# Kernel tuning notes

Measured on AMD Instinct MI355X. Metric: run time of the kernel, lower is better.

## Reference

```python
import jax, jax.numpy as jnp
import numpy as np

N_NODES = 50000
N_EDGES = 800000
IN_DIM = 128
OUT_DIM = 64


def setup_inputs() -> dict:
    key = jax.random.key(0)
    k1, k2, k3, k4, k5 = jax.random.split(key, 5)
    x = jax.random.normal(k1, (N_NODES, IN_DIM), dtype=jnp.float32)
    # Glorot-uniform-ish init for the GCN weight (weight_variable_glorot)
    limit = np.sqrt(6.0 / (IN_DIM + OUT_DIM)).astype(np.float32)
    weight = jax.random.uniform(k2, (IN_DIM, OUT_DIM), dtype=jnp.float32,
                                minval=-limit, maxval=limit)
    adj_row = jax.random.randint(k3, (N_EDGES,), 0, N_NODES, dtype=jnp.int32)
    adj_col = jax.random.randint(k4, (N_EDGES,), 0, N_NODES, dtype=jnp.int32)
    adj_val = jax.random.uniform(k5, (N_EDGES,), dtype=jnp.float32)
    return {"x": x, "weight": weight, "adj_row": adj_row,
            "adj_col": adj_col, "adj_val": adj_val}


def reference(x, weight, adj_row, adj_col, adj_val):
    # x: [N, F_in], weight: [F_in, F_out]; dropout=0.0 (default) is identity.
    xw = jnp.matmul(x, weight)                      # [N, F_out] dense GEMM
    # spmm(adj, xw) with adj in COO: gather neighbor feats, scale, scatter-add
    msg = adj_val[:, None] * xw[adj_col]            # [E, F_out]
    agg = jax.ops.segment_sum(msg, adj_row, num_segments=x.shape[0])  # [N, F_out]
    return jax.nn.relu(agg)
```

## Files before the change

kernel.cpp:

```cpp
#include <hip/hip_runtime.h>

#define IN_DIM 128
#define OUT_DIM 64
#define PADK 136
#define RB 128
#define RBSH 7
#define CAPB 2560
#define AB2 256

typedef float f32x4 __attribute__((ext_vector_type(4)));
typedef short bf16x8 __attribute__((ext_vector_type(8)));

__device__ __forceinline__ unsigned short f2bf(float f) {
    unsigned u = __float_as_uint(f);
    return (unsigned short)((u + 0x7FFFu + ((u >> 16) & 1u)) >> 16);
}
__device__ __forceinline__ float bf2f(unsigned short h) {
    return __uint_as_float((unsigned)h << 16);
}

__device__ __forceinline__ void gemm_body(const float* __restrict__ x,
                                          const float* __restrict__ w,
                                          unsigned short* __restrict__ xwb,
                                          int N, int blk,
                                          unsigned short* lds) {
    unsigned short* Bhi = lds;
    unsigned short* Blo = lds + 64 * PADK;

    const int t = threadIdx.x;
    const int r0 = blk * 64;

    {
        const int c = t >> 2;
        const int kb = (t & 3) * 32;
        for (int k4 = 0; k4 < 32; k4 += 4) {
            ushort4 h, l;
            float v0 = w[(kb + k4 + 0) * OUT_DIM + c];
            float v1 = w[(kb + k4 + 1) * OUT_DIM + c];
            float v2 = w[(kb + k4 + 2) * OUT_DIM + c];
            float v3 = w[(kb + k4 + 3) * OUT_DIM + c];
            h.x = f2bf(v0); l.x = f2bf(v0 - bf2f(h.x));
            h.y = f2bf(v1); l.y = f2bf(v1 - bf2f(h.y));
            h.z = f2bf(v2); l.z = f2bf(v2 - bf2f(h.z));
            h.w = f2bf(v3); l.w = f2bf(v3 - bf2f(h.w));
            *(ushort4*)&Bhi[c * PADK + kb + k4] = h;
            *(ushort4*)&Blo[c * PADK + kb + k4] = l;
        }
    }

    const int lane = t & 63;
    const int wv = t >> 6;
    const int m = lane & 15;
    const int quad = lane >> 4;

    int row = r0 + wv * 16 + m; if (row >= N) row = N - 1;
    const float4* xr = (const float4*)(x + (size_t)row * IN_DIM);
    bf16x8 ahi[4], alo[4];
#pragma unroll
    for (int ks = 0; ks < 4; ++ks) {
        const float4 v0 = xr[ks * 8 + quad * 2];
        const float4 v1 = xr[ks * 8 + quad * 2 + 1];
        float f[8] = {v0.x, v0.y, v0.z, v0.w, v1.x, v1.y, v1.z, v1.w};
        bf16x8 h8, l8;
#pragma unroll
        for (int i = 0; i < 8; ++i) {
            const unsigned short h = f2bf(f[i]);
            h8[i] = (short)h;
            l8[i] = (short)f2bf(f[i] - bf2f(h));
        }
        ahi[ks] = h8; alo[ks] = l8;
    }
    __syncthreads();

#pragma unroll
    for (int ct = 0; ct < 4; ++ct) {
        f32x4 acc = {0.f, 0.f, 0.f, 0.f};
#pragma unroll
        for (int ks = 0; ks < 4; ++ks) {
            const int off = (ct * 16 + m) * PADK + ks * 32 + quad * 8;
            bf16x8 bh = *(const bf16x8*)&Bhi[off];
            bf16x8 bl = *(const bf16x8*)&Blo[off];
            acc = __builtin_amdgcn_mfma_f32_16x16x32_bf16(alo[ks], bh, acc, 0, 0, 0);
            acc = __builtin_amdgcn_mfma_f32_16x16x32_bf16(ahi[ks], bl, acc, 0, 0, 0);
            acc = __builtin_amdgcn_mfma_f32_16x16x32_bf16(ahi[ks], bh, acc, 0, 0, 0);
        }
#pragma unroll
        for (int i = 0; i < 4; ++i) {
            const int r = r0 + wv * 16 + quad * 4 + i;
            if (r < N) xwb[(size_t)r * OUT_DIM + ct * 16 + m] = f2bf(acc[i]);
        }
    }
}

__device__ __forceinline__ void afill_body(
        const int* __restrict__ arow, const int* __restrict__ acol,
        const float* __restrict__ aval, int* __restrict__ pcur,
        int* __restrict__ ocount, uint4* __restrict__ olist,
        uint2* __restrict__ payload, int E, int NB, int chunk, int blk,
        int* ldsi) {
    int* cnt  = ldsi;
    int* base = ldsi + 512;
    const int t = threadIdx.x;
    const int lo = blk * chunk;
    const int hi = min(E, lo + chunk);
    if (lo >= hi) return;
    const int len = hi - lo;
    const int n4  = len >> 2;
    const int4*   ar4 = (const int4*)(arow + lo);
    const int4*   ac4 = (const int4*)(acol + lo);
    const float4* av4 = (const float4*)(aval + lo);

    for (int i = t; i < NB; i += 256) cnt[i] = 0;
    __syncthreads();

    for (int j = t; j < n4; j += 256) {
        const int4 r = ar4[j];
        atomicAdd(&cnt[r.x >> RBSH], 1);
        atomicAdd(&cnt[r.y >> RBSH], 1);
        atomicAdd(&cnt[r.z >> RBSH], 1);
        atomicAdd(&cnt[r.w >> RBSH], 1);
    }
    for (int e = lo + (n4 << 2) + t; e < hi; e += 256)
        atomicAdd(&cnt[arow[e] >> RBSH], 1);
    __syncthreads();

    for (int i = t; i < NB; i += 256) {
        const int c = cnt[i];
        base[i] = c ? atomicAdd(&pcur[i], c) : 0;
        cnt[i] = 0;
    }
    __syncthreads();

#define AF_EMIT(RR, CC, VV) do {                                              \
        const int b_ = (RR) >> RBSH;                                          \
        const int slot_ = base[b_] + atomicAdd(&cnt[b_], 1);                  \
        const unsigned w0_ = (unsigned)(CC) |                                 \
                             ((unsigned)((RR) & (RB - 1)) << 16);             \
        const unsigned w1_ = __float_as_uint(VV);                             \
        if (slot_ < CAPB) {                                                   \
            payload[(size_t)b_ * CAPB + slot_] = make_uint2(w0_, w1_);        \
        } else {                                                              \
            const int oi_ = atomicAdd(ocount, 1);                             \
            olist[oi_] = make_uint4((unsigned)(RR), (unsigned)(CC), w1_, 0u); \
        }                                                                     \
    } while (0)

    for (int j = t; j < n4; j += 256) {
        const int4   r = ar4[j];
        const int4   c = ac4[j];
        const float4 v = av4[j];
        AF_EMIT(r.x, c.x, v.x);
        AF_EMIT(r.y, c.y, v.y);
        AF_EMIT(r.z, c.z, v.z);
        AF_EMIT(r.w, c.w, v.w);
    }
    for (int e = lo + (n4 << 2) + t; e < hi; e += 256)
        AF_EMIT(arow[e], acol[e], aval[e]);
#undef AF_EMIT
}

__global__ __launch_bounds__(256) void gemm_afill(
        const float* __restrict__ x, const float* __restrict__ w,
        unsigned short* __restrict__ xwb, int N,
        const int* __restrict__ arow, const int* __restrict__ acol,
        const float* __restrict__ aval, int* __restrict__ pcur,
        int* __restrict__ ocount, uint4* __restrict__ olist,
        uint2* __restrict__ payload, int E, int NB, int chunk) {
    __shared__ unsigned short LB[2 * 64 * PADK];
    if ((int)blockIdx.x < AB2) {
        afill_body(arow, acol, aval, pcur, ocount, olist, payload, E, NB,
                   chunk, blockIdx.x, (int*)LB);
    } else {
        gemm_body(x, w, xwb, N, blockIdx.x - AB2, LB);
    }
}

__global__ __launch_bounds__(256) void gemm_only(const float* __restrict__ x,
                                                 const float* __restrict__ w,
                                                 unsigned short* __restrict__ xwb,
                                                 int N) {
    __shared__ unsigned short LB[2 * 64 * PADK];
    gemm_body(x, w, xwb, N, blockIdx.x, LB);
}

__global__ __launch_bounds__(512) void bagg6(
        const int* __restrict__ pcur, const uint2* __restrict__ payload,
        const unsigned short* __restrict__ xwb, float* __restrict__ out, int N,
        const int* __restrict__ ocount, const uint4* __restrict__ olist) {
    __shared__ uint2 stage[CAPB];
    __shared__ int binc[RB];
    __shared__ int bins[RB + 1];
    __shared__ int pl[RB];
    __shared__ int hsum[2];
    const int t = threadIdx.x;
    const int lane = t & 63;
    const int wv = t >> 6;
    const int b = blockIdx.x;
    const int r0 = b << RBSH;

    const int cnt = min(pcur[b], CAPB);
    if (t < RB) { binc[t] = 0; pl[t] = 0; }
    __syncthreads();

    const uint2* pay = payload + (size_t)b * CAPB;
    for (int i = t; i < cnt; i += 512)
        atomicAdd(&binc[(pay[i].x >> 16) & (RB - 1)], 1);
    __syncthreads();

    int s = 0;
    if (t < RB) {
        s = binc[t];
#pragma unroll
        for (int d = 1; d < 64; d <<= 1) {
            const int u = __shfl_up(s, d, 64);
            if (lane >= d) s += u;
        }
        if (lane == 63) hsum[t >> 6] = s;
    }
    __syncthreads();
    if (t < RB) {
        bins[t + 1] = s + (t >= 64 ? hsum[0] : 0);
        if (t == 0) bins[0] = 0;
    }
    __syncthreads();

    for (int i = t; i < cnt; i += 512) {
        const uint2 e = pay[i];
        const int rl = (e.x >> 16) & (RB - 1);
        stage[bins[rl] + atomicAdd(&pl[rl], 1)] = e;
    }
    __syncthreads();

    float acc[16];
#pragma unroll
    for (int lr = 0; lr < 16; ++lr) {
        const int row = wv * 16 + lr;
        int j = bins[row];
        const int end = bins[row + 1];
        float a0 = 0.f, a1 = 0.f;
        for (; j + 8 <= end; j += 8) {
            uint2 e0 = stage[j],   e1 = stage[j+1], e2 = stage[j+2], e3 = stage[j+3];
            uint2 e4 = stage[j+4], e5 = stage[j+5], e6 = stage[j+6], e7 = stage[j+7];
            float g0 = bf2f(xwb[(size_t)(e0.x & 0xFFFF) * OUT_DIM + lane]);
            float g1 = bf2f(xwb[(size_t)(e1.x & 0xFFFF) * OUT_DIM + lane]);
            float g2 = bf2f(xwb[(size_t)(e2.x & 0xFFFF) * OUT_DIM + lane]);
            float g3 = bf2f(xwb[(size_t)(e3.x & 0xFFFF) * OUT_DIM + lane]);
            float g4 = bf2f(xwb[(size_t)(e4.x & 0xFFFF) * OUT_DIM + lane]);
            float g5 = bf2f(xwb[(size_t)(e5.x & 0xFFFF) * OUT_DIM + lane]);
            float g6 = bf2f(xwb[(size_t)(e6.x & 0xFFFF) * OUT_DIM + lane]);
            float g7 = bf2f(xwb[(size_t)(e7.x & 0xFFFF) * OUT_DIM + lane]);
            a0 = fmaf(__uint_as_float(e0.y), g0, a0);
            a1 = fmaf(__uint_as_float(e1.y), g1, a1);
            a0 = fmaf(__uint_as_float(e2.y), g2, a0);
            a1 = fmaf(__uint_as_float(e3.y), g3, a1);
            a0 = fmaf(__uint_as_float(e4.y), g4, a0);
            a1 = fmaf(__uint_as_float(e5.y), g5, a1);
            a0 = fmaf(__uint_as_float(e6.y), g6, a0);
            a1 = fmaf(__uint_as_float(e7.y), g7, a1);
        }
        for (; j + 4 <= end; j += 4) {
            uint2 e0 = stage[j], e1 = stage[j+1], e2 = stage[j+2], e3 = stage[j+3];
            float g0 = bf2f(xwb[(size_t)(e0.x & 0xFFFF) * OUT_DIM + lane]);
            float g1 = bf2f(xwb[(size_t)(e1.x & 0xFFFF) * OUT_DIM + lane]);
            float g2 = bf2f(xwb[(size_t)(e2.x & 0xFFFF) * OUT_DIM + lane]);
            float g3 = bf2f(xwb[(size_t)(e3.x & 0xFFFF) * OUT_DIM + lane]);
            a0 = fmaf(__uint_as_float(e0.y), g0, a0);
            a1 = fmaf(__uint_as_float(e1.y), g1, a1);
            a0 = fmaf(__uint_as_float(e2.y), g2, a0);
            a1 = fmaf(__uint_as_float(e3.y), g3, a1);
        }
        for (; j < end; ++j) {
            uint2 e0 = stage[j];
            a0 = fmaf(__uint_as_float(e0.y),
                      bf2f(xwb[(size_t)(e0.x & 0xFFFF) * OUT_DIM + lane]), a0);
        }
        acc[lr] = a0 + a1;
    }

    const int oc = *ocount;
    for (int i = 0; i < oc; ++i) {
        const uint4 e = olist[i];
        const int lr = (int)e.x - r0 - wv * 16;
        if (lr >= 0 && lr < 16)
            acc[lr] += __uint_as_float(e.z) *
                       bf2f(xwb[(size_t)e.y * OUT_DIM + lane]);
    }

#pragma unroll
    for (int lr = 0; lr < 16; ++lr) {
        const int row = r0 + wv * 16 + lr;
        if (row < N) {
            const float v = acc[lr];
            out[(size_t)row * OUT_DIM + lane] = v > 0.f ? v : 0.f;
        }
    }
}

__global__ __launch_bounds__(256) void scatter_edges(
        const int* __restrict__ arow, const int* __restrict__ acol,
        const float* __restrict__ aval, const unsigned short* __restrict__ xwb,
        float* __restrict__ out, int E) {
    const int lane = threadIdx.x & 63;
    int gw = (blockIdx.x * 256 + (int)threadIdx.x) >> 6;
    const int nw = (gridDim.x * 256) >> 6;
    for (int e = gw; e < E; e += nw) {
        const float m = aval[e] * bf2f(xwb[(size_t)acol[e] * OUT_DIM + lane]);
        atomicAdd(&out[(size_t)arow[e] * OUT_DIM + lane], m);
    }
}

__global__ __launch_bounds__(256) void relu_inplace(float* __restrict__ o, int n4) {
    float4* p = (float4*)o;
    int i = blockIdx.x * 256 + threadIdx.x;
    const int stride = gridDim.x * 256;
    for (; i < n4; i += stride) {
        float4 v = p[i];
        v.x = v.x > 0.f ? v.x : 0.f;
        v.y = v.y > 0.f ? v.y : 0.f;
        v.z = v.z > 0.f ? v.z : 0.f;
        v.w = v.w > 0.f ? v.w : 0.f;
        p[i] = v;
    }
}

static inline size_t align256(size_t x) { return (x + 255) & ~(size_t)255; }

extern "C" void kernel_launch(void* const* d_in, const int* in_sizes, int n_in,
                              void* d_out, int out_size, void* d_ws, size_t ws_size,
                              hipStream_t stream) {
    const float* x    = (const float*)d_in[0];
    const float* w    = (const float*)d_in[1];
    const int*   arow = (const int*)d_in[2];
    const int*   acol = (const int*)d_in[3];
    const float* aval = (const float*)d_in[4];
    float*       out  = (float*)d_out;

    const int N  = in_sizes[0] / IN_DIM;
    const int E  = in_sizes[2];
    const int NB = (N + RB - 1) >> RBSH;
    const int GB = (N + 63) / 64;

    char* ws = (char*)d_ws;
    const size_t szXW  = align256((size_t)N * OUT_DIM * sizeof(unsigned short));
    const size_t szCnt = align256((size_t)(NB + 1) * sizeof(int));
    const size_t szOl  = align256((size_t)E * sizeof(uint4));
    const size_t szPay = (size_t)NB * CAPB * sizeof(uint2);
    const size_t need0 = szXW + szCnt + szOl + szPay;

    unsigned short* xwb = (unsigned short*)ws;
    int*   pcur    = (int*)(ws + szXW);
    int*   ocount  = pcur + NB;
    uint4* olist   = (uint4*)(ws + szXW + szCnt);
    uint2* payload = (uint2*)(ws + szXW + szCnt + szOl);

    if (ws_size >= need0 && N <= 65536 && NB <= 512) {
        (void)hipMemsetAsync(pcur, 0, (size_t)(NB + 1) * sizeof(int), stream);
        const int chunk = (((E + AB2 - 1) / AB2) + 3) & ~3;
        gemm_afill<<<AB2 + GB, 256, 0, stream>>>(x, w, xwb, N, arow, acol, aval,
                                                 pcur, ocount, olist, payload,
                                                 E, NB, chunk);
        bagg6<<<NB, 512, 0, stream>>>(pcur, payload, xwb, out, N, ocount, olist);
    } else {
        gemm_only<<<GB, 256, 0, stream>>>(x, w, xwb, N);
        (void)hipMemsetAsync(d_out, 0, (size_t)out_size * sizeof(float), stream);
        scatter_edges<<<4096, 256, 0, stream>>>(arow, acol, aval, xwb, out, E);
        relu_inplace<<<2048, 256, 0, stream>>>(out, out_size / 4);
    }
}
```

Measured before the change: 131.5 us.

## Replace global bucket cursors with per-block fixed-capacity bucket slots

Edge binning no longer reserves global slots through atomics on a shared per-bucket cursor. Each fill block writes into its own fixed slice of 32 entries per row bucket and records its per-bucket counts. The aggregation kernel loads the whole 128x32 tile into LDS in one bulk copy and filters out unused slots before its local sort. This removes the counting pass and the global atomics, and the number of fill blocks is halved. In exchange the payload grows, LDS use doubles, and any bucket slice that overflows spills to the slower overflow list.

```diff
diff --git a/kernel.cpp b/kernel.cpp
--- a/kernel.cpp
+++ b/kernel.cpp
@@ -5,8 +5,9 @@
 #define PADK 136
 #define RB 128
 #define RBSH 7
-#define CAPB 2560
-#define AB2 256
+#define AB2 128
+#define CAP 32
+#define STAGE 4096
 
 typedef float f32x4 __attribute__((ext_vector_type(4)));
 typedef short bf16x8 __attribute__((ext_vector_type(8)));
@@ -94,81 +95,66 @@
 
 __device__ __forceinline__ void afill_body(
         const int* __restrict__ arow, const int* __restrict__ acol,
-        const float* __restrict__ aval, int* __restrict__ pcur,
+        const float* __restrict__ aval, int* __restrict__ cnts,
         int* __restrict__ ocount, uint4* __restrict__ olist,
         uint2* __restrict__ payload, int E, int NB, int chunk, int blk,
         int* ldsi) {
-    int* cnt  = ldsi;
-    int* base = ldsi + 512;
+    int* cnt = ldsi;
     const int t = threadIdx.x;
+    for (int i = t; i < NB; i += 256) cnt[i] = 0;
+    __syncthreads();
+
     const int lo = blk * chunk;
     const int hi = min(E, lo + chunk);
-    if (lo >= hi) return;
-    const int len = hi - lo;
-    const int n4  = len >> 2;
-    const int4*   ar4 = (const int4*)(arow + lo);
-    const int4*   ac4 = (const int4*)(acol + lo);
-    const float4* av4 = (const float4*)(aval + lo);
-
-    for (int i = t; i < NB; i += 256) cnt[i] = 0;
-    __syncthreads();
-
-    for (int j = t; j < n4; j += 256) {
-        const int4 r = ar4[j];
-        atomicAdd(&cnt[r.x >> RBSH], 1);
-        atomicAdd(&cnt[r.y >> RBSH], 1);
-        atomicAdd(&cnt[r.z >> RBSH], 1);
-        atomicAdd(&cnt[r.w >> RBSH], 1);
-    }
-    for (int e = lo + (n4 << 2) + t; e < hi; e += 256)
-        atomicAdd(&cnt[arow[e] >> RBSH], 1);
-    __syncthreads();
-
-    for (int i = t; i < NB; i += 256) {
-        const int c = cnt[i];
-        base[i] = c ? atomicAdd(&pcur[i], c) : 0;
-        cnt[i] = 0;
-    }
-    __syncthreads();
+    if (lo < hi) {
+        const int len = hi - lo;
+        const int n4  = len >> 2;
+        const int4*   ar4 = (const int4*)(arow + lo);
+        const int4*   ac4 = (const int4*)(acol + lo);
+        const float4* av4 = (const float4*)(aval + lo);
 
 #define AF_EMIT(RR, CC, VV) do {                                              \
         const int b_ = (RR) >> RBSH;                                          \
-        const int slot_ = base[b_] + atomicAdd(&cnt[b_], 1);                  \
+        const int slot_ = atomicAdd(&cnt[b_], 1);                             \
         const unsigned w0_ = (unsigned)(CC) |                                 \
                              ((unsigned)((RR) & (RB - 1)) << 16);             \
         const unsigned w1_ = __float_as_uint(VV);                             \
-        if (slot_ < CAPB) {                                                   \
-            payload[(size_t)b_ * CAPB + slot_] = make_uint2(w0_, w1_);        \
+        if (slot_ < CAP) {                                                    \
+            payload[((size_t)b_ * AB2 + blk) * CAP + slot_] =                 \
+                make_uint2(w0_, w1_);                                         \
         } else {                                                              \
             const int oi_ = atomicAdd(ocount, 1);                             \
             olist[oi_] = make_uint4((unsigned)(RR), (unsigned)(CC), w1_, 0u); \
         }                                                                     \
     } while (0)
 
-    for (int j = t; j < n4; j += 256) {
-        const int4   r = ar4[j];
-        const int4   c = ac4[j];
-        const float4 v = av4[j];
-        AF_EMIT(r.x, c.x, v.x);
-        AF_EMIT(r.y, c.y, v.y);
-        AF_EMIT(r.z, c.z, v.z);
-        AF_EMIT(r.w, c.w, v.w);
-    }
-    for (int e = lo + (n4 << 2) + t; e < hi; e += 256)
-        AF_EMIT(arow[e], acol[e], aval[e]);
+        for (int j = t; j < n4; j += 256) {
+            const int4   r = ar4[j];
+            const int4   c = ac4[j];
+            const float4 v = av4[j];
+            AF_EMIT(r.x, c.x, v.x);
+            AF_EMIT(r.y, c.y, v.y);
+            AF_EMIT(r.z, c.z, v.z);
+            AF_EMIT(r.w, c.w, v.w);
+        }
+        for (int e = lo + (n4 << 2) + t; e < hi; e += 256)
+            AF_EMIT(arow[e], acol[e], aval[e]);
 #undef AF_EMIT
+    }
+    __syncthreads();
+    for (int i = t; i < NB; i += 256) cnts[i * AB2 + blk] = cnt[i];
 }
 
 __global__ __launch_bounds__(256) void gemm_afill(
         const float* __restrict__ x, const float* __restrict__ w,
         unsigned short* __restrict__ xwb, int N,
         const int* __restrict__ arow, const int* __restrict__ acol,
-        const float* __restrict__ aval, int* __restrict__ pcur,
+        const float* __restrict__ aval, int* __restrict__ cnts,
         int* __restrict__ ocount, uint4* __restrict__ olist,
         uint2* __restrict__ payload, int E, int NB, int chunk) {
     __shared__ unsigned short LB[2 * 64 * PADK];
     if ((int)blockIdx.x < AB2) {
-        afill_body(arow, acol, aval, pcur, ocount, olist, payload, E, NB,
+        afill_body(arow, acol, aval, cnts, ocount, olist, payload, E, NB,
                    chunk, blockIdx.x, (int*)LB);
     } else {
         gemm_body(x, w, xwb, N, blockIdx.x - AB2, LB);
@@ -183,11 +169,13 @@
     gemm_body(x, w, xwb, N, blockIdx.x, LB);
 }
 
-__global__ __launch_bounds__(512) void bagg6(
-        const int* __restrict__ pcur, const uint2* __restrict__ payload,
+__global__ __launch_bounds__(512) void bagg7(
+        const int* __restrict__ cnts, const uint2* __restrict__ payload,
         const unsigned short* __restrict__ xwb, float* __restrict__ out, int N,
         const int* __restrict__ ocount, const uint4* __restrict__ olist) {
-    __shared__ uint2 stage[CAPB];
+    __shared__ uint2 raw[STAGE];
+    __shared__ uint2 stage[STAGE];
+    __shared__ int scnt[AB2];
     __shared__ int binc[RB];
     __shared__ int bins[RB + 1];
     __shared__ int pl[RB];
@@ -198,13 +186,15 @@
     const int b = blockIdx.x;
     const int r0 = b << RBSH;
 
-    const int cnt = min(pcur[b], CAPB);
+    if (t < AB2) scnt[t] = min(cnts[b * AB2 + t], CAP);
     if (t < RB) { binc[t] = 0; pl[t] = 0; }
-    __syncthreads();
-
-    const uint2* pay = payload + (size_t)b * CAPB;
-    for (int i = t; i < cnt; i += 512)
-        atomicAdd(&binc[(pay[i].x >> 16) & (RB - 1)], 1);
+    const uint2* src = payload + (size_t)b * AB2 * CAP;
+    for (int i = t; i < STAGE; i += 512) raw[i] = src[i];
+    __syncthreads();
+
+    for (int i = t; i < STAGE; i += 512)
+        if ((i & (CAP - 1)) < scnt[i >> 5])
+            atomicAdd(&binc[(raw[i].x >> 16) & (RB - 1)], 1);
     __syncthreads();
 
     int s = 0;
@@ -224,10 +214,12 @@
     }
     __syncthreads();
 
-    for (int i = t; i < cnt; i += 512) {
-        const uint2 e = pay[i];
-        const int rl = (e.x >> 16) & (RB - 1);
-        stage[bins[rl] + atomicAdd(&pl[rl], 1)] = e;
+    for (int i = t; i < STAGE; i += 512) {
+        if ((i & (CAP - 1)) < scnt[i >> 5]) {
+            const uint2 e = raw[i];
+            const int rl = (e.x >> 16) & (RB - 1);
+            stage[bins[rl] + atomicAdd(&pl[rl], 1)] = e;
+        }
     }
     __syncthreads();
 
@@ -342,24 +334,24 @@
 
     char* ws = (char*)d_ws;
     const size_t szXW  = align256((size_t)N * OUT_DIM * sizeof(unsigned short));
-    const size_t szCnt = align256((size_t)(NB + 1) * sizeof(int));
+    const size_t szCnt = align256(((size_t)NB * AB2 + 1) * sizeof(int));
     const size_t szOl  = align256((size_t)E * sizeof(uint4));
-    const size_t szPay = (size_t)NB * CAPB * sizeof(uint2);
+    const size_t szPay = (size_t)NB * AB2 * CAP * sizeof(uint2);
     const size_t need0 = szXW + szCnt + szOl + szPay;
 
     unsigned short* xwb = (unsigned short*)ws;
-    int*   pcur    = (int*)(ws + szXW);
-    int*   ocount  = pcur + NB;
+    int*   cnts    = (int*)(ws + szXW);
+    int*   ocount  = cnts + (size_t)NB * AB2;
     uint4* olist   = (uint4*)(ws + szXW + szCnt);
     uint2* payload = (uint2*)(ws + szXW + szCnt + szOl);
 
-    if (ws_size >= need0 && N <= 65536 && NB <= 512) {
-        (void)hipMemsetAsync(pcur, 0, (size_t)(NB + 1) * sizeof(int), stream);
+    if (ws_size >= need0 && N <= 65536 && NB <= 1024) {
+        (void)hipMemsetAsync(ocount, 0, sizeof(int), stream);
         const int chunk = (((E + AB2 - 1) / AB2) + 3) & ~3;
         gemm_afill<<<AB2 + GB, 256, 0, stream>>>(x, w, xwb, N, arow, acol, aval,
-                                                 pcur, ocount, olist, payload,
+                                                 cnts, ocount, olist, payload,
                                                  E, NB, chunk);
-        bagg6<<<NB, 512, 0, stream>>>(pcur, payload, xwb, out, N, ocount, olist);
+        bagg7<<<NB, 512, 0, stream>>>(cnts, payload, xwb, out, N, ocount, olist);
     } else {
         gemm_only<<<GB, 256, 0, stream>>>(x, w, xwb, N);
         (void)hipMemsetAsync(d_out, 0, (size_t)out_size * sizeof(float), stream);
```

Result: no change. 133.3 us (+1.3%).
